# Kernel optimization log

Measured on AMD Instinct MI355X. Metric: run time of the kernel, lower is better.

The kernel has to match this reference:

```python
import jax, jax.numpy as jnp
import numpy as np

N_BITS = 3        # routing dims (slice_mask = first 3 indices)
N_HEADS = 8       # 2**N_BITS
D_FEAT = 512      # input_dim - N_BITS
D_BASE = 1024     # base MLP output
D_HEAD_H = 1024   # head hidden
D_OUT = 512       # head output
BATCH = 8192


def setup_inputs() -> dict:
    key = jax.random.key(0)
    ks = jax.random.split(key, 8)
    s = lambda fan_in: 1.0 / np.sqrt(fan_in)
    x = jax.random.normal(ks[0], (BATCH, N_BITS + D_FEAT), dtype=jnp.float32)
    Wb = jax.random.normal(ks[1], (D_FEAT, D_BASE), dtype=jnp.float32) * s(D_FEAT)
    bb = jax.random.normal(ks[2], (D_BASE,), dtype=jnp.float32) * s(D_FEAT)
    Wh1 = jax.random.normal(ks[3], (N_HEADS, D_BASE, D_HEAD_H), dtype=jnp.float32) * s(D_BASE)
    bh1 = jax.random.normal(ks[4], (N_HEADS, D_HEAD_H), dtype=jnp.float32) * s(D_BASE)
    Wh2 = jax.random.normal(ks[5], (N_HEADS, D_HEAD_H, D_OUT), dtype=jnp.float32) * s(D_HEAD_H)
    bh2 = jax.random.normal(ks[6], (N_HEADS, D_OUT), dtype=jnp.float32) * s(D_HEAD_H)
    return {"x": x, "Wb": Wb, "bb": bb, "Wh1": Wh1, "bh1": bh1, "Wh2": Wh2, "bh2": bh2}


def _combs():
    # Faithful to the torch `recursive` construction for three single-index
    # binary slices: combs[bit, head] = (head >> bit) & 1
    return ((jnp.arange(N_HEADS)[None, :] >> jnp.arange(N_BITS)[:, None]) & 1).astype(bool)


def reference(x, Wb, bb, Wh1, bh1, Wh2, bh2):
    bits = x[:, :N_BITS] > 0.5          # [B, 3] routing bits
    feat = x[:, N_BITS:]                # [B, 512]
    base = jax.nn.relu(feat @ Wb + bb)  # [B, 1024] shared base net
    # all heads run over the full batch (as in the original module)
    h = jax.nn.relu(jnp.einsum('bd,hde->bhe', base, Wh1) + bh1[None])  # [B, 8, 1024]
    out_all = jnp.einsum('bhe,heo->bho', h, Wh2) + bh2[None]           # [B, 8, 512]
    combs = _combs()                                                   # [3, 8]
    sel = jnp.all(bits[:, :, None] == combs[None], axis=1).astype(x.dtype)  # [B, 8] one-hot
    return jnp.einsum('bho,bh->bo', out_all, sel)                      # [B, 512]
```

## Files before the change

kernel.cpp:

```cpp
#include <hip/hip_runtime.h>
#include <hip/hip_bf16.h>
#include <stdint.h>

using short8 = __attribute__((ext_vector_type(8))) short;
using f32x4  = __attribute__((ext_vector_type(4))) float;

#define NBITS 3
#define NHEADS 8
#define BATCH 8192
#define DFEAT 512
#define DBASE 1024
#define DHH   1024
#define DOUT  512
#define XCOLS (NBITS + DFEAT)

static __device__ __forceinline__ unsigned short f2bf(float f) {
    union { float f; unsigned u; } v; v.f = f;
    unsigned r = v.u + 0x7FFFu + ((v.u >> 16) & 1u);
    return (unsigned short)(r >> 16);
}

__global__ void k_bucket(const float* __restrict__ x, int* __restrict__ cnt,
                         int* __restrict__ rows) {
    int r = blockIdx.x * 256 + threadIdx.x;
    if (r >= BATCH) return;
    const float* xr = x + (size_t)r * XCOLS;
    int h = (xr[0] > 0.5f ? 1 : 0) | (xr[1] > 0.5f ? 2 : 0) | (xr[2] > 0.5f ? 4 : 0);
    int slot = atomicAdd(cnt + h, 1);
    rows[h * BATCH + slot] = r;
}

__global__ void k_feat(const float* __restrict__ x, unsigned short* __restrict__ feat) {
    int t = blockIdx.x * 256 + threadIdx.x;
    int row = t >> 6, c8 = (t & 63) << 3;
    const float* src = x + (size_t)row * XCOLS + NBITS + c8;
    short8 v;
#pragma unroll
    for (int i = 0; i < 8; ++i) v[i] = (short)f2bf(src[i]);
    *(short8*)(feat + (size_t)row * DFEAT + c8) = v;
}

__global__ void k_transpose(const float* __restrict__ W, unsigned short* __restrict__ WT,
                            int K, int N) {
    __shared__ float tile[32][33];
    int b  = blockIdx.z;
    int n0 = blockIdx.x << 5, k0 = blockIdx.y << 5;
    int tx = threadIdx.x & 31, ty = threadIdx.x >> 5;
    const float* Wb = W + (size_t)b * K * N;
    unsigned short* WTb = WT + (size_t)b * K * N;
#pragma unroll
    for (int j = 0; j < 32; j += 8)
        tile[ty + j][tx] = Wb[(size_t)(k0 + ty + j) * N + n0 + tx];
    __syncthreads();
#pragma unroll
    for (int j = 0; j < 32; j += 8)
        WTb[(size_t)(n0 + ty + j) * K + k0 + tx] = f2bf(tile[tx][ty + j]);
}

template<bool GATHER, bool RELU, bool OUTBF16, int NF>
__global__ __launch_bounds__(512, 1)
void k_gemm3(const unsigned short* __restrict__ A, int lda, int K,
             const unsigned short* __restrict__ BT,
             const float* __restrict__ bias,
             void* __restrict__ C, int ldc,
             const int* __restrict__ rowsAll, const int* __restrict__ cntAll,
             int Nfull, int nshift) {
    constexpr int BN  = NF * 64;
    constexpr int BNB = BN * 128;
    constexpr int NB  = BNB / 8192;

    const int bid  = blockIdx.x;
    const int mt   = bid & 63;
    const int nt   = (bid >> 6) & ((1 << nshift) - 1);
    const int head = GATHER ? (bid >> (6 + nshift)) : 0;
    const int m0 = mt * 128;
    const int n0 = nt * BN;
    int M = BATCH;
    const int* rows = nullptr;
    if (GATHER) {
        M = cntAll[head];
        if (m0 >= M) return;
        rows = rowsAll + head * BATCH;
    }
    const unsigned short* BTh = BT + (size_t)head * Nfull * K;
    const float* biash = bias + (size_t)head * Nfull;

    __shared__ __align__(16) char lds[3 * 16384 + 3 * BNB];
    char* ldsA = lds;
    char* ldsB = lds + 3 * 16384;

    const int t    = threadIdx.x;
    const int w    = t >> 6;
    const int lane = t & 63;
    const int wr = w >> 2, wc = w & 3;
    const int ln = lane & 15, lq = lane >> 4;

    const unsigned short* gA[2];
    {
        int rl  = t >> 3;
        int kch = (t & 7) ^ (rl & 7);
#pragma unroll
        for (int h = 0; h < 2; ++h) {
            int idx = m0 + h * 64 + rl;
            int r;
            if (GATHER) { idx = idx < M ? idx : (M - 1); r = rows[idx]; }
            else r = idx;
            gA[h] = A + (size_t)r * lda + kch * 8;
        }
    }
    const unsigned short* gB[NB];
#pragma unroll
    for (int i = 0; i < NB; ++i) {
        int c   = i * 512 + t;
        int cl  = c >> 3;
        int kch = (c & 7) ^ (cl & 7);
        gB[i] = BTh + (size_t)(n0 + cl) * K + kch * 8;
    }

#define STAGE(kt_, d_)                                                                     \
    { _Pragma("unroll") for (int h = 0; h < 2; ++h)                                        \
        __builtin_amdgcn_global_load_lds(                                                  \
            (const __attribute__((address_space(1))) void*)(gA[h] + (kt_) * 64),           \
            (__attribute__((address_space(3))) void*)(ldsA + (d_) * 16384 + h * 8192 + w * 1024), \
            16, 0, 0);                                                                     \
      _Pragma("unroll") for (int i = 0; i < NB; ++i)                                       \
        __builtin_amdgcn_global_load_lds(                                                  \
            (const __attribute__((address_space(1))) void*)(gB[i] + (kt_) * 64),           \
            (__attribute__((address_space(3))) void*)(ldsB + (d_) * BNB + i * 8192 + w * 1024), \
            16, 0, 0); }

#define WAITV_STEADY()                                                                     \
    { if constexpr (NF == 4) asm volatile("s_waitcnt vmcnt(12)" ::: "memory");             \
      else                   asm volatile("s_waitcnt vmcnt(8)"  ::: "memory"); }

    f32x4 acc[4][NF] = {};
    const int NT = K >> 6;

    STAGE(0, 0);
    STAGE(1, 1);

    for (int kt = 0; kt < NT; ++kt) {
        const int bc = kt % 3;
        const int bs = (kt + 2) % 3;
        const int ks = (kt + 2 < NT) ? kt + 2 : NT - 1;
        STAGE(ks, bs);
        WAITV_STEADY();
        __builtin_amdgcn_s_barrier();
        const char* cA = ldsA + bc * 16384;
        const char* cB = ldsB + bc * BNB;
#pragma unroll
        for (int ksl = 0; ksl < 2; ++ksl) {
            short8 af[4], bf[NF];
#pragma unroll
            for (int m = 0; m < 4; ++m) {
                int rA = wr * 64 + m * 16 + ln;
                int ch = ((ksl << 2) | lq) ^ (ln & 7);
                af[m] = *(const short8*)(cA + rA * 128 + ch * 16);
            }
#pragma unroll
            for (int n = 0; n < NF; ++n) {
                int cBc = wc * (NF * 16) + n * 16 + ln;
                int ch  = ((ksl << 2) | lq) ^ (ln & 7);
                bf[n] = *(const short8*)(cB + cBc * 128 + ch * 16);
            }
            __builtin_amdgcn_s_setprio(1);
#pragma unroll
            for (int m = 0; m < 4; ++m)
#pragma unroll
                for (int n = 0; n < NF; ++n)
                    acc[m][n] = __builtin_amdgcn_mfma_f32_16x16x32_bf16(af[m], bf[n], acc[m][n], 0, 0, 0);
            __builtin_amdgcn_s_setprio(0);
        }
        __builtin_amdgcn_s_barrier();
    }
#undef STAGE
#undef WAITV_STEADY

#pragma unroll
    for (int n = 0; n < NF; ++n) {
        int col = n0 + wc * (NF * 16) + n * 16 + ln;
        float bv = biash[col];
#pragma unroll
        for (int m = 0; m < 4; ++m) {
#pragma unroll
            for (int j = 0; j < 4; ++j) {
                int rt = wr * 64 + m * 16 + lq * 4 + j;
                int grow;
                if (GATHER) {
                    if (m0 + rt >= M) continue;
                    grow = rows[m0 + rt];
                } else {
                    grow = m0 + rt;
                }
                float v = acc[m][n][j] + bv;
                if (RELU) v = fmaxf(v, 0.0f);
                if (OUTBF16)
                    ((unsigned short*)C)[(size_t)grow * ldc + col] = f2bf(v);
                else
                    ((float*)C)[(size_t)grow * ldc + col] = v;
            }
        }
    }
}

extern "C" void kernel_launch(void* const* d_in, const int* in_sizes, int n_in,
                              void* d_out, int out_size, void* d_ws, size_t ws_size,
                              hipStream_t stream) {
    const float* x   = (const float*)d_in[0];
    const float* Wb  = (const float*)d_in[1];
    const float* bb  = (const float*)d_in[2];
    const float* Wh1 = (const float*)d_in[3];
    const float* bh1 = (const float*)d_in[4];
    const float* Wh2 = (const float*)d_in[5];
    const float* bh2 = (const float*)d_in[6];

    char* ws = (char*)d_ws;
    unsigned short* feat = (unsigned short*)(ws);
    unsigned short* WbT  = (unsigned short*)(ws + (8ull  << 20));
    unsigned short* Wh1T = (unsigned short*)(ws + (9ull  << 20));
    unsigned short* Wh2T = (unsigned short*)(ws + (25ull << 20));
    unsigned short* base = (unsigned short*)(ws + (33ull << 20));
    unsigned short* hbuf = (unsigned short*)(ws + (49ull << 20));
    int* rows            = (int*)(ws + (65ull << 20));
    int* cnt             = (int*)(ws + (65ull << 20) + (256ull << 10));

    hipMemsetAsync(cnt, 0, NHEADS * sizeof(int), stream);
    k_bucket<<<BATCH / 256, 256, 0, stream>>>(x, cnt, rows);
    k_feat<<<(BATCH * 64) / 256, 256, 0, stream>>>(x, feat);
    k_transpose<<<dim3(DBASE / 32, DFEAT / 32, 1), 256, 0, stream>>>(Wb, WbT, DFEAT, DBASE);
    k_transpose<<<dim3(DHH / 32, DBASE / 32, NHEADS), 256, 0, stream>>>(Wh1, Wh1T, DBASE, DHH);
    k_transpose<<<dim3(DOUT / 32, DHH / 32, NHEADS), 256, 0, stream>>>(Wh2, Wh2T, DHH, DOUT);

    k_gemm3<false, true, true, 4><<<256, 512, 0, stream>>>(
        feat, DFEAT, DFEAT, WbT, bb, base, DBASE, nullptr, nullptr, DBASE, 2);
    k_gemm3<true, true, true, 4><<<2048, 512, 0, stream>>>(
        base, DBASE, DBASE, Wh1T, bh1, hbuf, DHH, rows, cnt, DHH, 2);
    k_gemm3<true, false, false, 2><<<2048, 512, 0, stream>>>(
        hbuf, DHH, DHH, Wh2T, bh2, d_out, DOUT, rows, cnt, DOUT, 2);
}
```

Measured before the change: 349.2 us.

## Replace GEMM with 64-row tiles reading B fragments directly from global

The 128xBN GEMM with 512 threads and triple-buffered A and B in LDS is replaced by a 64-row tile kernel using 256 threads, two blocks per CU, and a double-buffered 256-wide K chunk of A only. Each wave now loads its B (weight) fragments straight from global memory into registers instead of staging them through LDS. The aim is to raise occupancy, cut LDS traffic, and use fewer barriers per K step. The cost is that B is no longer shared across waves or rows through LDS, so weight reads depend on L2 and are not prefetched, and global-load latency may stall the MFMAs.

```diff
diff --git a/kernel.cpp b/kernel.cpp
--- a/kernel.cpp
+++ b/kernel.cpp
@@ -58,22 +58,19 @@
 }
 
 template<bool GATHER, bool RELU, bool OUTBF16, int NF>
-__global__ __launch_bounds__(512, 1)
-void k_gemm3(const unsigned short* __restrict__ A, int lda, int K,
+__global__ __launch_bounds__(256, 2)
+void k_gemmd(const unsigned short* __restrict__ A, int lda, int K,
              const unsigned short* __restrict__ BT,
              const float* __restrict__ bias,
              void* __restrict__ C, int ldc,
              const int* __restrict__ rowsAll, const int* __restrict__ cntAll,
              int Nfull, int nshift) {
-    constexpr int BN  = NF * 64;
-    constexpr int BNB = BN * 128;
-    constexpr int NB  = BNB / 8192;
-
+    constexpr int BN = NF * 16 * 4;
     const int bid  = blockIdx.x;
-    const int mt   = bid & 63;
-    const int nt   = (bid >> 6) & ((1 << nshift) - 1);
-    const int head = GATHER ? (bid >> (6 + nshift)) : 0;
-    const int m0 = mt * 128;
+    const int mt   = bid & 127;
+    const int nt   = (bid >> 7) & ((1 << nshift) - 1);
+    const int head = GATHER ? (bid >> (7 + nshift)) : 0;
+    const int m0 = mt * 64;
     const int n0 = nt * BN;
     int M = BATCH;
     const int* rows = nullptr;
@@ -85,106 +82,83 @@
     const unsigned short* BTh = BT + (size_t)head * Nfull * K;
     const float* biash = bias + (size_t)head * Nfull;
 
-    __shared__ __align__(16) char lds[3 * 16384 + 3 * BNB];
-    char* ldsA = lds;
-    char* ldsB = lds + 3 * 16384;
+    __shared__ __align__(16) char lds[2 * 32768];
 
     const int t    = threadIdx.x;
     const int w    = t >> 6;
     const int lane = t & 63;
-    const int wr = w >> 2, wc = w & 3;
     const int ln = lane & 15, lq = lane >> 4;
-
-    const unsigned short* gA[2];
-    {
-        int rl  = t >> 3;
-        int kch = (t & 7) ^ (rl & 7);
-#pragma unroll
-        for (int h = 0; h < 2; ++h) {
-            int idx = m0 + h * 64 + rl;
-            int r;
-            if (GATHER) { idx = idx < M ? idx : (M - 1); r = rows[idx]; }
-            else r = idx;
-            gA[h] = A + (size_t)r * lda + kch * 8;
-        }
-    }
-    const unsigned short* gB[NB];
-#pragma unroll
-    for (int i = 0; i < NB; ++i) {
-        int c   = i * 512 + t;
-        int cl  = c >> 3;
-        int kch = (c & 7) ^ (cl & 7);
-        gB[i] = BTh + (size_t)(n0 + cl) * K + kch * 8;
-    }
-
-#define STAGE(kt_, d_)                                                                     \
-    { _Pragma("unroll") for (int h = 0; h < 2; ++h)                                        \
+    const int r7 = ln & 7;
+
+    const unsigned short* gsrc[8];
+#pragma unroll
+    for (int i = 0; i < 8; ++i) {
+        int r  = i * 8 + (t >> 5);
+        int lg = (t & 31) ^ (r & 7);
+        int gr;
+        if (GATHER) { int idx = m0 + r; idx = idx < M ? idx : M - 1; gr = rows[idx]; }
+        else gr = m0 + r;
+        gsrc[i] = A + (size_t)gr * lda + lg * 8;
+    }
+    const unsigned short* gb[NF];
+#pragma unroll
+    for (int n = 0; n < NF; ++n) {
+        int col = n0 + w * (NF * 16) + n * 16 + ln;
+        gb[n] = BTh + (size_t)col * K + lq * 8;
+    }
+    const int dstw = w * 1024;
+
+#define STAGEQ(cq_, d_)                                                                    \
+    { _Pragma("unroll") for (int i = 0; i < 8; ++i)                                        \
         __builtin_amdgcn_global_load_lds(                                                  \
-            (const __attribute__((address_space(1))) void*)(gA[h] + (kt_) * 64),           \
-            (__attribute__((address_space(3))) void*)(ldsA + (d_) * 16384 + h * 8192 + w * 1024), \
-            16, 0, 0);                                                                     \
-      _Pragma("unroll") for (int i = 0; i < NB; ++i)                                       \
-        __builtin_amdgcn_global_load_lds(                                                  \
-            (const __attribute__((address_space(1))) void*)(gB[i] + (kt_) * 64),           \
-            (__attribute__((address_space(3))) void*)(ldsB + (d_) * BNB + i * 8192 + w * 1024), \
+            (const __attribute__((address_space(1))) void*)(gsrc[i] + (cq_) * 256),        \
+            (__attribute__((address_space(3))) void*)(lds + (d_) * 32768 + i * 4096 + dstw), \
             16, 0, 0); }
 
-#define WAITV_STEADY()                                                                     \
-    { if constexpr (NF == 4) asm volatile("s_waitcnt vmcnt(12)" ::: "memory");             \
-      else                   asm volatile("s_waitcnt vmcnt(8)"  ::: "memory"); }
-
     f32x4 acc[4][NF] = {};
-    const int NT = K >> 6;
-
-    STAGE(0, 0);
-    STAGE(1, 1);
-
-    for (int kt = 0; kt < NT; ++kt) {
-        const int bc = kt % 3;
-        const int bs = (kt + 2) % 3;
-        const int ks = (kt + 2 < NT) ? kt + 2 : NT - 1;
-        STAGE(ks, bs);
-        WAITV_STEADY();
-        __builtin_amdgcn_s_barrier();
-        const char* cA = ldsA + bc * 16384;
-        const char* cB = ldsB + bc * BNB;
-#pragma unroll
-        for (int ksl = 0; ksl < 2; ++ksl) {
+    const int NC = K >> 8;
+
+    STAGEQ(0, 0);
+    __syncthreads();
+
+    for (int cq = 0; cq < NC; ++cq) {
+        const int d = cq & 1;
+        if (cq + 1 < NC) STAGEQ(cq + 1, d ^ 1);
+        const char* cA = lds + d * 32768;
+        const unsigned short* bq[NF];
+#pragma unroll
+        for (int n = 0; n < NF; ++n) bq[n] = gb[n] + cq * 256;
+#pragma unroll
+        for (int ks = 0; ks < 8; ++ks) {
             short8 af[4], bf[NF];
 #pragma unroll
             for (int m = 0; m < 4; ++m) {
-                int rA = wr * 64 + m * 16 + ln;
-                int ch = ((ksl << 2) | lq) ^ (ln & 7);
-                af[m] = *(const short8*)(cA + rA * 128 + ch * 16);
+                int row  = m * 16 + ln;
+                int phys = ((ks * 4) | lq) ^ r7;
+                af[m] = *(const short8*)(cA + row * 512 + phys * 16);
             }
 #pragma unroll
-            for (int n = 0; n < NF; ++n) {
-                int cBc = wc * (NF * 16) + n * 16 + ln;
-                int ch  = ((ksl << 2) | lq) ^ (ln & 7);
-                bf[n] = *(const short8*)(cB + cBc * 128 + ch * 16);
-            }
-            __builtin_amdgcn_s_setprio(1);
+            for (int n = 0; n < NF; ++n)
+                bf[n] = *(const short8*)(bq[n] + ks * 32);
 #pragma unroll
             for (int m = 0; m < 4; ++m)
 #pragma unroll
                 for (int n = 0; n < NF; ++n)
                     acc[m][n] = __builtin_amdgcn_mfma_f32_16x16x32_bf16(af[m], bf[n], acc[m][n], 0, 0, 0);
-            __builtin_amdgcn_s_setprio(0);
         }
-        __builtin_amdgcn_s_barrier();
-    }
-#undef STAGE
-#undef WAITV_STEADY
+        __syncthreads();
+    }
+#undef STAGEQ
 
 #pragma unroll
     for (int n = 0; n < NF; ++n) {
-        int col = n0 + wc * (NF * 16) + n * 16 + ln;
+        int col = n0 + w * (NF * 16) + n * 16 + ln;
         float bv = biash[col];
 #pragma unroll
         for (int m = 0; m < 4; ++m) {
 #pragma unroll
             for (int j = 0; j < 4; ++j) {
-                int rt = wr * 64 + m * 16 + lq * 4 + j;
+                int rt = m * 16 + lq * 4 + j;
                 int grow;
                 if (GATHER) {
                     if (m0 + rt >= M) continue;
@@ -231,10 +205,10 @@
     k_transpose<<<dim3(DHH / 32, DBASE / 32, NHEADS), 256, 0, stream>>>(Wh1, Wh1T, DBASE, DHH);
     k_transpose<<<dim3(DOUT / 32, DHH / 32, NHEADS), 256, 0, stream>>>(Wh2, Wh2T, DHH, DOUT);
 
-    k_gemm3<false, true, true, 4><<<256, 512, 0, stream>>>(
+    k_gemmd<false, true, true, 4><<<512, 256, 0, stream>>>(
         feat, DFEAT, DFEAT, WbT, bb, base, DBASE, nullptr, nullptr, DBASE, 2);
-    k_gemm3<true, true, true, 4><<<2048, 512, 0, stream>>>(
+    k_gemmd<true, true, true, 4><<<4096, 256, 0, stream>>>(
         base, DBASE, DBASE, Wh1T, bh1, hbuf, DHH, rows, cnt, DHH, 2);
-    k_gemm3<true, false, false, 2><<<2048, 512, 0, stream>>>(
+    k_gemmd<true, false, false, 2><<<4096, 256, 0, stream>>>(
         hbuf, DHH, DHH, Wh2T, bh2, d_out, DOUT, rows, cnt, DOUT, 2);
 }
```

After: 354.9 us. Within noise of the previous version (+1.6%).
